# Kernel optimization log

Hardware: AMD Instinct MI355X
Metric: run time of the kernel (lower is better)

The kernel has to match this reference:

```python
import jax, jax.numpy as jnp
import numpy as np

IN_FEATURES = 4096
OUT_FEATURES = 8192
LUT_SIZE = 65536  # 256 * 256 two-level codebook


def setup_inputs() -> dict:
    key = jax.random.key(0)
    k_x, k_b, k_f, k_s, k_l = jax.random.split(key, 5)
    x = jax.random.normal(k_x, (2, 256, IN_FEATURES), dtype=jnp.float32)
    base_idx = jax.random.randint(k_b, (OUT_FEATURES, IN_FEATURES), 0, 256, dtype=jnp.int32)
    fine_idx = jax.random.randint(k_f, (OUT_FEATURES, IN_FEATURES), 0, 256, dtype=jnp.int32)
    scale = jax.random.uniform(k_s, (OUT_FEATURES, 1), dtype=jnp.float32)
    lut = jax.random.normal(k_l, (LUT_SIZE,), dtype=jnp.float32)
    return {"x": x, "base_idx": base_idx, "fine_idx": fine_idx, "scale": scale, "lut": lut}


def reference(x, base_idx, fine_idx, scale, lut):
    # Two-level LUT dequant: combined 16-bit index = base*256 + fine
    combined_idx = base_idx * 256 + fine_idx              # [out, in] int32
    weights = lut[combined_idx] * scale                   # [out, in] fp32, per-row scale
    # F.linear(x, weights) == x @ weights.T
    return jnp.einsum('bsi,oi->bso', x, weights)
```

## Files before the change

### kernel.cpp

```cpp
#include <hip/hip_runtime.h>

typedef unsigned short ushort_t;
typedef unsigned int   uint32;
typedef __attribute__((ext_vector_type(8))) short short8;
typedef __attribute__((ext_vector_type(4))) float floatx4;

#define IN_F   4096
#define OUT_F  8192
#define M_TOT  512
#define NB     32
#define BK     128
#define WS     136
#define NITER  (IN_F / BK)

__device__ __forceinline__ ushort_t f2bf(float f) {
    uint32 u = __builtin_bit_cast(uint32, f);
    u += 0x7FFFu + ((u >> 16) & 1u);
    return (ushort_t)(u >> 16);
}

__global__ void cvt_x_kernel(const float* __restrict__ x, ushort_t* __restrict__ xb) {
    int i = (blockIdx.x * 256 + threadIdx.x) * 8;
    float4 v0 = *(const float4*)(x + i);
    float4 v1 = *(const float4*)(x + i + 4);
    short8 s;
    s[0] = (short)f2bf(v0.x); s[1] = (short)f2bf(v0.y);
    s[2] = (short)f2bf(v0.z); s[3] = (short)f2bf(v0.w);
    s[4] = (short)f2bf(v1.x); s[5] = (short)f2bf(v1.y);
    s[6] = (short)f2bf(v1.z); s[7] = (short)f2bf(v1.w);
    *(short8*)(xb + i) = s;
}

template<bool XBF16>
__global__ __launch_bounds__(1024, 4)
void ghost_kernel(const float* __restrict__ xf, const ushort_t* __restrict__ xb,
                  const int* __restrict__ base_idx, const int* __restrict__ fine_idx,
                  const float* __restrict__ scale, const float* __restrict__ lut,
                  float* __restrict__ out)
{
    __shared__ ushort_t sh_lut[65536];
    __shared__ ushort_t sh_w[2][NB * WS];

    const int tid = threadIdx.x;
    const int n0  = blockIdx.x * NB;

    for (int i = tid * 4; i < 65536; i += 1024 * 4) {
        float4 v = *(const float4*)(lut + i);
        sh_lut[i + 0] = f2bf(v.x);
        sh_lut[i + 1] = f2bf(v.y);
        sh_lut[i + 2] = f2bf(v.z);
        sh_lut[i + 3] = f2bf(v.w);
    }

    const int sn  = tid >> 5;
    const int skq = (tid & 31) * 4;
    const int* bp = base_idx + (size_t)(n0 + sn) * IN_F + skq;
    const int* fp = fine_idx + (size_t)(n0 + sn) * IN_F + skq;

    __syncthreads();

    int4 pb = *(const int4*)(bp);
    int4 pf = *(const int4*)(fp);
    {
        uint32 w0 = (uint32)sh_lut[(pb.x << 8) + pf.x] | ((uint32)sh_lut[(pb.y << 8) + pf.y] << 16);
        uint32 w1 = (uint32)sh_lut[(pb.z << 8) + pf.z] | ((uint32)sh_lut[(pb.w << 8) + pf.w] << 16);
        uint2 wv; wv.x = w0; wv.y = w1;
        *(uint2*)&sh_w[0][sn * WS + skq] = wv;
    }
    pb = *(const int4*)(bp + BK);
    pf = *(const int4*)(fp + BK);
    __syncthreads();

    const int lane = tid & 63;
    const int wave = tid >> 6;
    const int l16  = lane & 15;
    const int quad = lane >> 4;

    floatx4 acc[2][2];
    const floatx4 zero = {0.f, 0.f, 0.f, 0.f};
    acc[0][0] = zero; acc[0][1] = zero; acc[1][0] = zero; acc[1][1] = zero;

    const int mrow = wave * 32 + l16;
    const ushort_t* xrow  = XBF16 ? (xb + (size_t)mrow * IN_F + quad * 8) : (const ushort_t*)nullptr;
    const float*    xrowf = XBF16 ? (const float*)nullptr : (xf + (size_t)mrow * IN_F + quad * 8);

    for (int t = 0; t < NITER; ++t) {
        const int k0 = t * BK;

        {
            uint32 w0 = (uint32)sh_lut[(pb.x << 8) + pf.x] | ((uint32)sh_lut[(pb.y << 8) + pf.y] << 16);
            uint32 w1 = (uint32)sh_lut[(pb.z << 8) + pf.z] | ((uint32)sh_lut[(pb.w << 8) + pf.w] << 16);
            uint2 wv; wv.x = w0; wv.y = w1;
            *(uint2*)&sh_w[(t + 1) & 1][sn * WS + skq] = wv;
        }
        {
            const int kk = (t + 2 < NITER ? t + 2 : NITER - 1) * BK;
            pb = *(const int4*)(bp + kk);
            pf = *(const int4*)(fp + kk);
        }

        const ushort_t* wb = sh_w[t & 1];
#pragma unroll
        for (int ks = 0; ks < 4; ++ks) {
            const int kk = k0 + ks * 32;
            short8 b0 = *(const short8*)&wb[l16        * WS + ks * 32 + quad * 8];
            short8 b1 = *(const short8*)&wb[(16 + l16) * WS + ks * 32 + quad * 8];
            short8 a0, a1;
            if (XBF16) {
                a0 = *(const short8*)(xrow + kk);
                a1 = *(const short8*)(xrow + (size_t)16 * IN_F + kk);
            } else {
                const float* p0 = xrowf + kk;
                const float* p1 = xrowf + (size_t)16 * IN_F + kk;
                float4 u0 = *(const float4*)p0, u1 = *(const float4*)(p0 + 4);
                float4 v0 = *(const float4*)p1, v1 = *(const float4*)(p1 + 4);
                a0[0] = (short)f2bf(u0.x); a0[1] = (short)f2bf(u0.y);
                a0[2] = (short)f2bf(u0.z); a0[3] = (short)f2bf(u0.w);
                a0[4] = (short)f2bf(u1.x); a0[5] = (short)f2bf(u1.y);
                a0[6] = (short)f2bf(u1.z); a0[7] = (short)f2bf(u1.w);
                a1[0] = (short)f2bf(v0.x); a1[1] = (short)f2bf(v0.y);
                a1[2] = (short)f2bf(v0.z); a1[3] = (short)f2bf(v0.w);
                a1[4] = (short)f2bf(v1.x); a1[5] = (short)f2bf(v1.y);
                a1[6] = (short)f2bf(v1.z); a1[7] = (short)f2bf(v1.w);
            }
            acc[0][0] = __builtin_amdgcn_mfma_f32_16x16x32_bf16(a0, b0, acc[0][0], 0, 0, 0);
            acc[0][1] = __builtin_amdgcn_mfma_f32_16x16x32_bf16(a0, b1, acc[0][1], 0, 0, 0);
            acc[1][0] = __builtin_amdgcn_mfma_f32_16x16x32_bf16(a1, b0, acc[1][0], 0, 0, 0);
            acc[1][1] = __builtin_amdgcn_mfma_f32_16x16x32_bf16(a1, b1, acc[1][1], 0, 0, 0);
        }
        __syncthreads();
    }

#pragma unroll
    for (int nf = 0; nf < 2; ++nf) {
        const int col = n0 + nf * 16 + l16;
        const float sc = scale[col];
#pragma unroll
        for (int f = 0; f < 2; ++f) {
            const int r0 = wave * 32 + f * 16 + quad * 4;
#pragma unroll
            for (int r = 0; r < 4; ++r) {
                out[(size_t)(r0 + r) * OUT_F + col] = acc[f][nf][r] * sc;
            }
        }
    }
}

extern "C" void kernel_launch(void* const* d_in, const int* in_sizes, int n_in,
                              void* d_out, int out_size, void* d_ws, size_t ws_size,
                              hipStream_t stream) {
    const float* x      = (const float*)d_in[0];
    const int*   bidx   = (const int*)d_in[1];
    const int*   fidx   = (const int*)d_in[2];
    const float* scale  = (const float*)d_in[3];
    const float* lut    = (const float*)d_in[4];
    float*       out    = (float*)d_out;

    const size_t xb_bytes = (size_t)M_TOT * IN_F * sizeof(ushort_t);
    if (ws_size >= xb_bytes) {
        ushort_t* xb = (ushort_t*)d_ws;
        cvt_x_kernel<<<1024, 256, 0, stream>>>(x, xb);
        ghost_kernel<true><<<OUT_F / NB, 1024, 0, stream>>>(x, xb, bidx, fidx, scale, lut, out);
    } else {
        ghost_kernel<false><<<OUT_F / NB, 1024, 0, stream>>>(x, nullptr, bidx, fidx, scale, lut, out);
    }
}
```

Baseline: 383.0 us.

## Split dequant into separate pass and use a tiled 32x32 MFMA GEMM

Replaces the fused dequant-plus-GEMM with three passes when workspace allows. A dequant kernel writes bf16 weights to workspace, and a 128x128-tile GEMM then uses global_load_lds and 32x32x16 MFMAs with far more reuse of x and weights than the 32-column fused tile. This trades an extra 64MB write and read of bf16 weights for a compute-efficient GEMM. It depends on the workspace being large enough, otherwise the old path runs.

```diff
diff --git a/kernel.cpp b/kernel.cpp
--- a/kernel.cpp
+++ b/kernel.cpp
@@ -2,16 +2,13 @@
 
 typedef unsigned short ushort_t;
 typedef unsigned int   uint32;
-typedef __attribute__((ext_vector_type(8))) short short8;
-typedef __attribute__((ext_vector_type(4))) float floatx4;
+typedef __attribute__((ext_vector_type(8)))  short short8;
+typedef __attribute__((ext_vector_type(4)))  float floatx4;
+typedef __attribute__((ext_vector_type(16))) float floatx16;
 
 #define IN_F   4096
 #define OUT_F  8192
 #define M_TOT  512
-#define NB     32
-#define BK     128
-#define WS     136
-#define NITER  (IN_F / BK)
 
 __device__ __forceinline__ ushort_t f2bf(float f) {
     uint32 u = __builtin_bit_cast(uint32, f);
@@ -31,6 +28,131 @@
     *(short8*)(xb + i) = s;
 }
 
+__global__ __launch_bounds__(1024, 4)
+void dequant_kernel(const int* __restrict__ base_idx, const int* __restrict__ fine_idx,
+                    const float* __restrict__ lut, ushort_t* __restrict__ wq)
+{
+    __shared__ ushort_t sh_lut[65536];
+    const int tid = threadIdx.x;
+    for (int i = tid * 4; i < 65536; i += 1024 * 4) {
+        float4 v = *(const float4*)(lut + i);
+        sh_lut[i + 0] = f2bf(v.x);
+        sh_lut[i + 1] = f2bf(v.y);
+        sh_lut[i + 2] = f2bf(v.z);
+        sh_lut[i + 3] = f2bf(v.w);
+    }
+    __syncthreads();
+
+    const int row = blockIdx.x * 32 + (tid >> 5);
+    const int k0  = (tid & 31) * 4;
+    const int* bp = base_idx + (size_t)row * IN_F + k0;
+    const int* fp = fine_idx + (size_t)row * IN_F + k0;
+    ushort_t*  op = wq       + (size_t)row * IN_F + k0;
+
+    int4 cb[4], cf[4];
+#pragma unroll
+    for (int u = 0; u < 4; ++u) {
+        cb[u] = *(const int4*)(bp + u * 128);
+        cf[u] = *(const int4*)(fp + u * 128);
+    }
+    for (int b = 0; b < 8; ++b) {
+        int4 nb[4], nf[4];
+        const int bn = (b + 1 < 8) ? b + 1 : b;
+#pragma unroll
+        for (int u = 0; u < 4; ++u) {
+            nb[u] = *(const int4*)(bp + (bn * 4 + u) * 128);
+            nf[u] = *(const int4*)(fp + (bn * 4 + u) * 128);
+        }
+#pragma unroll
+        for (int u = 0; u < 4; ++u) {
+            uint32 w0 = (uint32)sh_lut[(cb[u].x << 8) + cf[u].x]
+                      | ((uint32)sh_lut[(cb[u].y << 8) + cf[u].y] << 16);
+            uint32 w1 = (uint32)sh_lut[(cb[u].z << 8) + cf[u].z]
+                      | ((uint32)sh_lut[(cb[u].w << 8) + cf[u].w] << 16);
+            uint2 wv; wv.x = w0; wv.y = w1;
+            *(uint2*)(op + (size_t)(b * 4 + u) * 128) = wv;
+        }
+#pragma unroll
+        for (int u = 0; u < 4; ++u) { cb[u] = nb[u]; cf[u] = nf[u]; }
+    }
+}
+
+#define BK 128
+__global__ __launch_bounds__(256)
+void gemm_kernel(const ushort_t* __restrict__ xb, const ushort_t* __restrict__ wq,
+                 const float* __restrict__ scale, float* __restrict__ out)
+{
+    __shared__ ushort_t shA[128 * BK];
+    __shared__ ushort_t shB[128 * BK];
+
+    const int tid  = threadIdx.x;
+    const int wave = tid >> 6;
+    const int m0   = blockIdx.x * 128;
+    const int n0   = blockIdx.y * 128;
+
+    const ushort_t* aBase = xb + (size_t)(m0 + (tid >> 4)) * IN_F + (tid & 15) * 8;
+    const ushort_t* bBase = wq + (size_t)(n0 + (tid >> 4)) * IN_F + (tid & 15) * 8;
+    typedef __attribute__((address_space(3))) ushort_t lds_us;
+    typedef const __attribute__((address_space(1))) void gvoid;
+    lds_us* sA3 = (lds_us*)shA;
+    lds_us* sB3 = (lds_us*)shB;
+
+    const int lane = tid & 63;
+    const int l31  = lane & 31;
+    const int lhi  = lane >> 5;
+    const int qm   = wave & 1;
+    const int qn   = wave >> 1;
+
+    floatx16 acc[2][2];
+    const floatx16 z16 = {0.f,0.f,0.f,0.f,0.f,0.f,0.f,0.f,0.f,0.f,0.f,0.f,0.f,0.f,0.f,0.f};
+    acc[0][0] = z16; acc[0][1] = z16; acc[1][0] = z16; acc[1][1] = z16;
+
+    for (int kb = 0; kb < IN_F; kb += BK) {
+#pragma unroll
+        for (int i = 0; i < 8; ++i) {
+            __builtin_amdgcn_global_load_lds((gvoid*)(aBase + (size_t)i * 16 * IN_F + kb),
+                (__attribute__((address_space(3))) void*)(sA3 + i * 2048 + wave * 512),
+                16, 0, 0);
+            __builtin_amdgcn_global_load_lds((gvoid*)(bBase + (size_t)i * 16 * IN_F + kb),
+                (__attribute__((address_space(3))) void*)(sB3 + i * 2048 + wave * 512),
+                16, 0, 0);
+        }
+        __syncthreads();
+
+#pragma unroll
+        for (int ks = 0; ks < 8; ++ks) {
+            short8 a0 = *(const short8*)&shA[(qm * 64 +      l31) * BK + ks * 16 + lhi * 8];
+            short8 a1 = *(const short8*)&shA[(qm * 64 + 32 + l31) * BK + ks * 16 + lhi * 8];
+            short8 b0 = *(const short8*)&shB[(qn * 64 +      l31) * BK + ks * 16 + lhi * 8];
+            short8 b1 = *(const short8*)&shB[(qn * 64 + 32 + l31) * BK + ks * 16 + lhi * 8];
+            acc[0][0] = __builtin_amdgcn_mfma_f32_32x32x16_bf16(a0, b0, acc[0][0], 0, 0, 0);
+            acc[0][1] = __builtin_amdgcn_mfma_f32_32x32x16_bf16(a0, b1, acc[0][1], 0, 0, 0);
+            acc[1][0] = __builtin_amdgcn_mfma_f32_32x32x16_bf16(a1, b0, acc[1][0], 0, 0, 0);
+            acc[1][1] = __builtin_amdgcn_mfma_f32_32x32x16_bf16(a1, b1, acc[1][1], 0, 0, 0);
+        }
+        __syncthreads();
+    }
+
+#pragma unroll
+    for (int nt = 0; nt < 2; ++nt) {
+        const int col = n0 + qn * 64 + nt * 32 + l31;
+        const float sc = scale[col];
+#pragma unroll
+        for (int mt = 0; mt < 2; ++mt) {
+            const int rbase = m0 + qm * 64 + mt * 32 + 4 * lhi;
+#pragma unroll
+            for (int reg = 0; reg < 16; ++reg) {
+                const int row = rbase + (reg & 3) + 8 * (reg >> 2);
+                out[(size_t)row * OUT_F + col] = acc[mt][nt][reg] * sc;
+            }
+        }
+    }
+}
+
+#define NB  32
+#define FBK 128
+#define WS  136
+#define NITER (IN_F / FBK)
 template<bool XBF16>
 __global__ __launch_bounds__(1024, 4)
 void ghost_kernel(const float* __restrict__ xf, const ushort_t* __restrict__ xb,
@@ -40,25 +162,18 @@
 {
     __shared__ ushort_t sh_lut[65536];
     __shared__ ushort_t sh_w[2][NB * WS];
-
     const int tid = threadIdx.x;
     const int n0  = blockIdx.x * NB;
-
     for (int i = tid * 4; i < 65536; i += 1024 * 4) {
         float4 v = *(const float4*)(lut + i);
-        sh_lut[i + 0] = f2bf(v.x);
-        sh_lut[i + 1] = f2bf(v.y);
-        sh_lut[i + 2] = f2bf(v.z);
-        sh_lut[i + 3] = f2bf(v.w);
-    }
-
+        sh_lut[i + 0] = f2bf(v.x); sh_lut[i + 1] = f2bf(v.y);
+        sh_lut[i + 2] = f2bf(v.z); sh_lut[i + 3] = f2bf(v.w);
+    }
     const int sn  = tid >> 5;
     const int skq = (tid & 31) * 4;
     const int* bp = base_idx + (size_t)(n0 + sn) * IN_F + skq;
     const int* fp = fine_idx + (size_t)(n0 + sn) * IN_F + skq;
-
     __syncthreads();
-
     int4 pb = *(const int4*)(bp);
     int4 pf = *(const int4*)(fp);
     {
@@ -67,26 +182,21 @@
         uint2 wv; wv.x = w0; wv.y = w1;
         *(uint2*)&sh_w[0][sn * WS + skq] = wv;
     }
-    pb = *(const int4*)(bp + BK);
-    pf = *(const int4*)(fp + BK);
+    pb = *(const int4*)(bp + FBK);
+    pf = *(const int4*)(fp + FBK);
     __syncthreads();
-
     const int lane = tid & 63;
     const int wave = tid >> 6;
     const int l16  = lane & 15;
     const int quad = lane >> 4;
-
     floatx4 acc[2][2];
     const floatx4 zero = {0.f, 0.f, 0.f, 0.f};
     acc[0][0] = zero; acc[0][1] = zero; acc[1][0] = zero; acc[1][1] = zero;
-
     const int mrow = wave * 32 + l16;
     const ushort_t* xrow  = XBF16 ? (xb + (size_t)mrow * IN_F + quad * 8) : (const ushort_t*)nullptr;
     const float*    xrowf = XBF16 ? (const float*)nullptr : (xf + (size_t)mrow * IN_F + quad * 8);
-
     for (int t = 0; t < NITER; ++t) {
-        const int k0 = t * BK;
-
+        const int k0 = t * FBK;
         {
             uint32 w0 = (uint32)sh_lut[(pb.x << 8) + pf.x] | ((uint32)sh_lut[(pb.y << 8) + pf.y] << 16);
             uint32 w1 = (uint32)sh_lut[(pb.z << 8) + pf.z] | ((uint32)sh_lut[(pb.w << 8) + pf.w] << 16);
@@ -94,11 +204,10 @@
             *(uint2*)&sh_w[(t + 1) & 1][sn * WS + skq] = wv;
         }
         {
-            const int kk = (t + 2 < NITER ? t + 2 : NITER - 1) * BK;
+            const int kk = (t + 2 < NITER ? t + 2 : NITER - 1) * FBK;
             pb = *(const int4*)(bp + kk);
             pf = *(const int4*)(fp + kk);
         }
-
         const ushort_t* wb = sh_w[t & 1];
 #pragma unroll
         for (int ks = 0; ks < 4; ++ks) {
@@ -130,7 +239,6 @@
         }
         __syncthreads();
     }
-
 #pragma unroll
     for (int nf = 0; nf < 2; ++nf) {
         const int col = n0 + nf * 16 + l16;
@@ -157,10 +265,18 @@
     float*       out    = (float*)d_out;
 
     const size_t xb_bytes = (size_t)M_TOT * IN_F * sizeof(ushort_t);
-    if (ws_size >= xb_bytes) {
-        ushort_t* xb = (ushort_t*)d_ws;
-        cvt_x_kernel<<<1024, 256, 0, stream>>>(x, xb);
-        ghost_kernel<true><<<OUT_F / NB, 1024, 0, stream>>>(x, xb, bidx, fidx, scale, lut, out);
+    const size_t wq_bytes = (size_t)OUT_F * IN_F * sizeof(ushort_t);
+
+    if (ws_size >= xb_bytes + wq_bytes) {
+        ushort_t* xbuf = (ushort_t*)d_ws;
+        ushort_t* wbuf = (ushort_t*)((char*)d_ws + xb_bytes);
+        cvt_x_kernel<<<1024, 256, 0, stream>>>(x, xbuf);
+        dequant_kernel<<<256, 1024, 0, stream>>>(bidx, fidx, lut, wbuf);
+        gemm_kernel<<<dim3(4, 64), 256, 0, stream>>>(xbuf, wbuf, scale, out);
+    } else if (ws_size >= xb_bytes) {
+        ushort_t* xbuf = (ushort_t*)d_ws;
+        cvt_x_kernel<<<1024, 256, 0, stream>>>(x, xbuf);
+        ghost_kernel<true><<<OUT_F / NB, 1024, 0, stream>>>(x, xbuf, bidx, fidx, scale, lut, out);
     } else {
         ghost_kernel<false><<<OUT_F / NB, 1024, 0, stream>>>(x, nullptr, bidx, fidx, scale, lut, out);
     }
```

Result: slower. 470.9 us (+23.0%).
